# Kernel optimization log

Hardware: AMD Instinct MI355X
Metric: run time of the kernel (lower is better)

The kernel has to match this reference:

```python
import jax, jax.numpy as jnp
import numpy as np

T, E, IN_F, OUT_F = 16384, 8, 2048, 4096


def setup_inputs() -> dict:
    key = jax.random.key(0)
    k1, k2 = jax.random.split(key)
    input_tokens = jax.random.normal(k1, (T, IN_F), dtype=jnp.float32)
    # weight_stack[e] is [out_features, in_features]; forward does x_e @ W_e.T
    weight_stack = jax.random.normal(k2, (E, OUT_F, IN_F), dtype=jnp.float32) * (1.0 / np.sqrt(IN_F))
    # tokens are pre-sorted by expert; sizes must sum to total_tokens
    m_sizes = jnp.full((E,), T // E, dtype=jnp.int32)
    m_offsets = jnp.concatenate([
        jnp.zeros((1,), jnp.int32),
        jnp.cumsum(m_sizes)[:-1].astype(jnp.int32),
    ])
    return {
        "input_tokens": input_tokens,
        "weight_stack": weight_stack,
        "m_sizes": m_sizes,
        "m_offsets": m_offsets,
    }


def reference(input_tokens, weight_stack, m_sizes, m_offsets):
    # Grouped GEMM: for expert e, rows [off_e : off_e + m_e] of the output are
    #   input_tokens[off_e : off_e + m_e] @ weight_stack[e].T
    # lax.ragged_dot expects rhs of shape [groups, K, N]; weight_stack is [E, N, K],
    # so a stride-only swapaxes gives the logical transpose (no data movement),
    # mirroring the CUTLASS stride-based transpose avoidance.
    rhs = jnp.swapaxes(weight_stack, 1, 2)  # [E, in_features, out_features]
    out = jax.lax.ragged_dot(input_tokens, rhs, m_sizes)  # [T, out_features]
    return out
```

## Files before the change

kernel.cpp:

```cpp
#include <hip/hip_runtime.h>
#include <hip/hip_bf16.h>
#include <stdint.h>

#define T_TOK 16384
#define NEXP  8
#define KF    2048
#define NF    4096

#define BM  256
#define BN  256
#define BKT 64
#define KT  (KF / BKT)

typedef __bf16 bf16;
typedef __attribute__((ext_vector_type(8))) __bf16  bf16x8;
typedef __attribute__((ext_vector_type(4))) __bf16  bf16x4;
typedef __attribute__((ext_vector_type(4))) float   f32x4;

__device__ __forceinline__ void async_copy16(const void* g, void* l) {
  __builtin_amdgcn_global_load_lds(
      (const __attribute__((address_space(1))) void*)g,
      (__attribute__((address_space(3))) void*)l,
      16, 0, 0);
}

__global__ __launch_bounds__(256) void convert_f32_to_bf16(
    const float* __restrict__ in, bf16* __restrict__ out, int n8) {
  int i = blockIdx.x * 256 + threadIdx.x;
  if (i >= n8) return;
  const float4* p = (const float4*)(in + (size_t)i * 8);
  float4 a = p[0];
  float4 b = p[1];
  bf16x8 v;
  v[0] = (bf16)a.x; v[1] = (bf16)a.y; v[2] = (bf16)a.z; v[3] = (bf16)a.w;
  v[4] = (bf16)b.x; v[5] = (bf16)b.y; v[6] = (bf16)b.z; v[7] = (bf16)b.w;
  *(bf16x8*)(out + (size_t)i * 8) = v;
}

__global__ __launch_bounds__(512, 2) void grouped_gemm_8ph(
    const bf16* __restrict__ Xb, const bf16* __restrict__ Wb,
    const int* __restrict__ m_offsets, float* __restrict__ out)
{
  __shared__ bf16 As[2][BM * BKT];
  __shared__ bf16 Bs[2][BN * BKT];

  const int bid = blockIdx.x;
  const int swz = (bid & 7) * 128 + (bid >> 3);
  const int m0 = (swz >> 4) * BM;
  const int n0 = (swz & 15) * BN;

  int e = 0;
#pragma unroll
  for (int i = 1; i < NEXP; ++i)
    if (m0 >= m_offsets[i]) e = i;

  const int tid  = threadIdx.x;
  const int lane = tid & 63;
  const int wave = tid >> 6;
  const int wm = (wave >> 2) * 128;
  const int wn = (wave & 3) * 64;
  const int q  = lane >> 4;
  const int r  = lane & 15;

  const bf16* Ag = Xb + (size_t)m0 * KF;
  const bf16* Bg = Wb + ((size_t)e * NF + n0) * KF;

  const int crow = tid >> 3;
  const int cbs  = (((tid & 7) << 4) ^ ((crow & 7) << 4));

#define STAGE_A(BUF, H, TT) do {                                              \
    const bf16* _s = Ag + (size_t)((H) * 128 + crow) * KF + (TT) * BKT        \
                        + (cbs >> 1);                                         \
    char* _d = (char*)(&As[(BUF)][(H) * 128 * BKT]) + tid * 16;               \
    async_copy16(_s, _d);                                                     \
    async_copy16(_s + (size_t)64 * KF, _d + 8192);                            \
  } while (0)
#define STAGE_B(BUF, H, TT) do {                                              \
    const bf16* _s = Bg + (size_t)((H) * 128 + crow) * KF + (TT) * BKT        \
                        + (cbs >> 1);                                         \
    char* _d = (char*)(&Bs[(BUF)][(H) * 128 * BKT]) + tid * 16;               \
    async_copy16(_s, _d);                                                     \
    async_copy16(_s + (size_t)64 * KF, _d + 8192);                            \
  } while (0)

  f32x4 acc[8][4];
#pragma unroll
  for (int m = 0; m < 8; ++m)
#pragma unroll
    for (int n = 0; n < 4; ++n)
      acc[m][n] = (f32x4)0.0f;

  STAGE_A(0, 0, 0); STAGE_A(0, 1, 0); STAGE_B(0, 0, 0); STAGE_B(0, 1, 0);
  STAGE_B(1, 0, 1); STAGE_B(1, 1, 1); STAGE_A(1, 0, 1);
  asm volatile("s_waitcnt vmcnt(6)" ::: "memory");
  __builtin_amdgcn_s_barrier();
  __builtin_amdgcn_sched_barrier(0);

#pragma unroll 2
  for (int t = 0; t < KT; ++t) {
    const int buf = t & 1;
    const char* Ab = (const char*)&As[buf][0];
    const char* Bb = (const char*)&Bs[buf][0];
    bf16x8 b0[4], b1[4], al[4], ah[4];

#pragma unroll
    for (int n = 0; n < 4; ++n) {
      const int row = wn + n * 16 + r;
      b0[n] = *(const bf16x8*)(Bb + row * 128 + ((q * 16) ^ ((row & 7) << 4)));
    }
#pragma unroll
    for (int m = 0; m < 4; ++m) {
      const int row = wm + m * 16 + r;
      al[m] = *(const bf16x8*)(Ab + row * 128 + ((q * 16) ^ ((row & 7) << 4)));
    }
#pragma unroll
    for (int n = 0; n < 4; ++n) {
      const int row = wn + n * 16 + r;
      b1[n] = *(const bf16x8*)(Bb + row * 128 + ((64 + q * 16) ^ ((row & 7) << 4)));
    }
#pragma unroll
    for (int m = 0; m < 4; ++m) {
      const int row = wm + (4 + m) * 16 + r;
      ah[m] = *(const bf16x8*)(Ab + row * 128 + ((q * 16) ^ ((row & 7) << 4)));
    }
    if (t + 1 < KT) STAGE_A(buf ^ 1, 1, t + 1);
    __builtin_amdgcn_s_barrier();
    asm volatile("s_waitcnt lgkmcnt(0)" ::: "memory");
    __builtin_amdgcn_sched_barrier(0);
    __builtin_amdgcn_s_setprio(1);
#pragma unroll
    for (int m = 0; m < 4; ++m)
#pragma unroll
      for (int n = 0; n < 4; ++n)
        acc[m][n] = __builtin_amdgcn_mfma_f32_16x16x32_bf16(
            al[m], b0[n], acc[m][n], 0, 0, 0);
    __builtin_amdgcn_s_setprio(0);
    __builtin_amdgcn_s_barrier();

    if (t + 2 < KT) STAGE_B(buf, 0, t + 2);
    __builtin_amdgcn_s_barrier();
    __builtin_amdgcn_sched_barrier(0);
    __builtin_amdgcn_s_setprio(1);
#pragma unroll
    for (int m = 0; m < 4; ++m)
#pragma unroll
      for (int n = 0; n < 4; ++n)
        acc[4 + m][n] = __builtin_amdgcn_mfma_f32_16x16x32_bf16(
            ah[m], b0[n], acc[4 + m][n], 0, 0, 0);
    __builtin_amdgcn_s_setprio(0);
    __builtin_amdgcn_s_barrier();

#pragma unroll
    for (int m = 0; m < 4; ++m) {
      const int row = wm + m * 16 + r;
      al[m] = *(const bf16x8*)(Ab + row * 128 + ((64 + q * 16) ^ ((row & 7) << 4)));
    }
#pragma unroll
    for (int m = 0; m < 4; ++m) {
      const int row = wm + (4 + m) * 16 + r;
      ah[m] = *(const bf16x8*)(Ab + row * 128 + ((64 + q * 16) ^ ((row & 7) << 4)));
    }
    if (t + 2 < KT) STAGE_B(buf, 1, t + 2);
    __builtin_amdgcn_s_barrier();
    asm volatile("s_waitcnt lgkmcnt(0)" ::: "memory");
    __builtin_amdgcn_sched_barrier(0);
    __builtin_amdgcn_s_setprio(1);
#pragma unroll
    for (int m = 0; m < 4; ++m)
#pragma unroll
      for (int n = 0; n < 4; ++n)
        acc[m][n] = __builtin_amdgcn_mfma_f32_16x16x32_bf16(
            al[m], b1[n], acc[m][n], 0, 0, 0);
    __builtin_amdgcn_s_setprio(0);
    __builtin_amdgcn_s_barrier();

    if (t + 2 < KT) STAGE_A(buf, 0, t + 2);
    __builtin_amdgcn_s_barrier();
    __builtin_amdgcn_sched_barrier(0);
    __builtin_amdgcn_s_setprio(1);
#pragma unroll
    for (int m = 0; m < 4; ++m)
#pragma unroll
      for (int n = 0; n < 4; ++n)
        acc[4 + m][n] = __builtin_amdgcn_mfma_f32_16x16x32_bf16(
            ah[m], b1[n], acc[4 + m][n], 0, 0, 0);
    __builtin_amdgcn_s_setprio(0);
    if (t + 1 < KT) {
      if (t + 2 < KT) { asm volatile("s_waitcnt vmcnt(6)" ::: "memory"); }
      else            { asm volatile("s_waitcnt vmcnt(0)" ::: "memory"); }
      __builtin_amdgcn_s_barrier();
      __builtin_amdgcn_sched_barrier(0);
    }
  }
#undef STAGE_A
#undef STAGE_B

#pragma unroll
  for (int m = 0; m < 8; ++m) {
#pragma unroll
    for (int n = 0; n < 4; ++n) {
      const int col = n0 + wn + n * 16 + r;
#pragma unroll
      for (int rr = 0; rr < 4; ++rr) {
        const int row = m0 + wm + m * 16 + q * 4 + rr;
        out[(size_t)row * NF + col] = acc[m][n][rr];
      }
    }
  }
}

template <bool PRE>
__global__ __launch_bounds__(256) void grouped_gemm_bt(
    const float* __restrict__ Xf, const bf16* __restrict__ Xb,
    const float* __restrict__ Wf, const bf16* __restrict__ Wb,
    const int* __restrict__ m_offsets,
    float* __restrict__ out)
{
  __shared__ bf16 As[128 * 32];
  __shared__ bf16 Bs[128 * 32];

  const int n0 = blockIdx.x * 128;
  const int m0 = blockIdx.y * 128;

  int e = 0;
#pragma unroll
  for (int i = 1; i < NEXP; ++i)
    if (m0 >= m_offsets[i]) e = i;

  const int tid  = threadIdx.x;
  const int lane = tid & 63;
  const int wave = tid >> 6;
  const int wm = (wave >> 1) * 64;
  const int wn = (wave & 1) * 64;
  const int q  = lane >> 4;
  const int r  = lane & 15;

  f32x4 acc[4][4];
#pragma unroll
  for (int im = 0; im < 4; ++im)
#pragma unroll
    for (int in = 0; in < 4; ++in)
      acc[im][in] = (f32x4)0.0f;

  const float* Af = Xf + (size_t)m0 * KF;
  const float* Bf = Wf + ((size_t)e * NF + n0) * KF;

  for (int kt = 0; kt < KF / 32; ++kt) {
#pragma unroll
    for (int i = 0; i < 4; ++i) {
      int f   = (i * 256 + tid) * 4;
      int row = f >> 5;
      int kel = f & 31;
      float4 av = *(const float4*)(Af + (size_t)row * KF + kt * 32 + kel);
      float4 bv = *(const float4*)(Bf + (size_t)row * KF + kt * 32 + kel);
      bf16x4 a4, b4;
      a4[0] = (bf16)av.x; a4[1] = (bf16)av.y; a4[2] = (bf16)av.z; a4[3] = (bf16)av.w;
      b4[0] = (bf16)bv.x; b4[1] = (bf16)bv.y; b4[2] = (bf16)bv.z; b4[3] = (bf16)bv.w;
      *(bf16x4*)(As + f) = a4;
      *(bf16x4*)(Bs + f) = b4;
    }
    __syncthreads();

    bf16x8 afr[4], bfr[4];
#pragma unroll
    for (int im = 0; im < 4; ++im)
      afr[im] = *(const bf16x8*)&As[(wm + im * 16 + r) * 32 + q * 8];
#pragma unroll
    for (int in = 0; in < 4; ++in)
      bfr[in] = *(const bf16x8*)&Bs[(wn + in * 16 + r) * 32 + q * 8];

#pragma unroll
    for (int im = 0; im < 4; ++im)
#pragma unroll
      for (int in = 0; in < 4; ++in)
        acc[im][in] = __builtin_amdgcn_mfma_f32_16x16x32_bf16(
            afr[im], bfr[in], acc[im][in], 0, 0, 0);

    __syncthreads();
  }

#pragma unroll
  for (int im = 0; im < 4; ++im) {
#pragma unroll
    for (int in = 0; in < 4; ++in) {
      int col = n0 + wn + in * 16 + r;
#pragma unroll
      for (int rr = 0; rr < 4; ++rr) {
        int row = m0 + wm + im * 16 + q * 4 + rr;
        out[(size_t)row * NF + col] = acc[im][in][rr];
      }
    }
  }
}

extern "C" void kernel_launch(void* const* d_in, const int* in_sizes, int n_in,
                              void* d_out, int out_size, void* d_ws, size_t ws_size,
                              hipStream_t stream) {
  const float* X         = (const float*)d_in[0];
  const float* W         = (const float*)d_in[1];
  const int*   m_offsets = (const int*)d_in[3];
  float*       out       = (float*)d_out;

  const size_t xElems = (size_t)T_TOK * KF;
  const size_t wElems = (size_t)NEXP * NF * KF;
  const size_t needed = (xElems + wElems) * sizeof(bf16);

  if (ws_size >= needed) {
    bf16* Xb = (bf16*)d_ws;
    bf16* Wb = (bf16*)((char*)d_ws + xElems * sizeof(bf16));
    int n8x = (int)(xElems / 8);
    int n8w = (int)(wElems / 8);
    convert_f32_to_bf16<<<n8x / 256, 256, 0, stream>>>(X, Xb, n8x);
    convert_f32_to_bf16<<<n8w / 256, 256, 0, stream>>>(W, Wb, n8w);
    dim3 grid((T_TOK / BM) * (NF / BN));
    grouped_gemm_8ph<<<grid, 512, 0, stream>>>(Xb, Wb, m_offsets, out);
  } else {
    dim3 grid(NF / 128, T_TOK / 128);
    grouped_gemm_bt<false><<<grid, 256, 0, stream>>>(
        X, nullptr, W, nullptr, m_offsets, out);
  }
}
```

Measured before the change: 807.8 us.

## Restructure GEMM main loop to cut barriers and overlap LDS reads with MFMA

Reworks the software pipeline of the bf16 grouped GEMM kernel. It removes most per-phase workgroup barriers, uses partial lgkmcnt waits so LDS fragment loads for the next phase overlap the current MFMA block, and regroups the async global-to-LDS staging: both A halves are issued early, both B halves after one barrier. The goal is less barrier stall and better latency hiding. The risk is LDS hazards, since fewer barriers protect buffer reuse, plus different register pressure. The fallback f32 kernel is only renamed, with the template removed.

```diff
diff --git a/kernel.cpp b/kernel.cpp
--- a/kernel.cpp
+++ b/kernel.cpp
@@ -37,7 +37,7 @@
   *(bf16x8*)(out + (size_t)i * 8) = v;
 }
 
-__global__ __launch_bounds__(512, 2) void grouped_gemm_8ph(
+__global__ __launch_bounds__(512, 2) void grouped_gemm_pipe(
     const bf16* __restrict__ Xb, const bf16* __restrict__ Wb,
     const int* __restrict__ m_offsets, float* __restrict__ out)
 {
@@ -91,8 +91,8 @@
       acc[m][n] = (f32x4)0.0f;
 
   STAGE_A(0, 0, 0); STAGE_A(0, 1, 0); STAGE_B(0, 0, 0); STAGE_B(0, 1, 0);
-  STAGE_B(1, 0, 1); STAGE_B(1, 1, 1); STAGE_A(1, 0, 1);
-  asm volatile("s_waitcnt vmcnt(6)" ::: "memory");
+  STAGE_B(1, 0, 1); STAGE_B(1, 1, 1);
+  asm volatile("s_waitcnt vmcnt(4)" ::: "memory");
   __builtin_amdgcn_s_barrier();
   __builtin_amdgcn_sched_barrier(0);
 
@@ -101,7 +101,7 @@
     const int buf = t & 1;
     const char* Ab = (const char*)&As[buf][0];
     const char* Bb = (const char*)&Bs[buf][0];
-    bf16x8 b0[4], b1[4], al[4], ah[4];
+    bf16x8 b0[4], b1[4], a0[4], a1[4];
 
 #pragma unroll
     for (int n = 0; n < 4; ++n) {
@@ -111,8 +111,9 @@
 #pragma unroll
     for (int m = 0; m < 4; ++m) {
       const int row = wm + m * 16 + r;
-      al[m] = *(const bf16x8*)(Ab + row * 128 + ((q * 16) ^ ((row & 7) << 4)));
-    }
+      a0[m] = *(const bf16x8*)(Ab + row * 128 + ((q * 16) ^ ((row & 7) << 4)));
+    }
+    __builtin_amdgcn_sched_barrier(0);
 #pragma unroll
     for (int n = 0; n < 4; ++n) {
       const int row = wn + n * 16 + r;
@@ -120,12 +121,12 @@
     }
 #pragma unroll
     for (int m = 0; m < 4; ++m) {
-      const int row = wm + (4 + m) * 16 + r;
-      ah[m] = *(const bf16x8*)(Ab + row * 128 + ((q * 16) ^ ((row & 7) << 4)));
-    }
-    if (t + 1 < KT) STAGE_A(buf ^ 1, 1, t + 1);
-    __builtin_amdgcn_s_barrier();
-    asm volatile("s_waitcnt lgkmcnt(0)" ::: "memory");
+      const int row = wm + 64 + m * 16 + r;
+      a1[m] = *(const bf16x8*)(Ab + row * 128 + ((q * 16) ^ ((row & 7) << 4)));
+    }
+    if (t + 1 < KT) { STAGE_A(buf ^ 1, 0, t + 1); STAGE_A(buf ^ 1, 1, t + 1); }
+
+    asm volatile("s_waitcnt lgkmcnt(8)" ::: "memory");
     __builtin_amdgcn_sched_barrier(0);
     __builtin_amdgcn_s_setprio(1);
 #pragma unroll
@@ -133,12 +134,16 @@
 #pragma unroll
       for (int n = 0; n < 4; ++n)
         acc[m][n] = __builtin_amdgcn_mfma_f32_16x16x32_bf16(
-            al[m], b0[n], acc[m][n], 0, 0, 0);
+            a0[m], b0[n], acc[m][n], 0, 0, 0);
     __builtin_amdgcn_s_setprio(0);
-    __builtin_amdgcn_s_barrier();
-
-    if (t + 2 < KT) STAGE_B(buf, 0, t + 2);
-    __builtin_amdgcn_s_barrier();
+    __builtin_amdgcn_sched_barrier(0);
+
+#pragma unroll
+    for (int m = 0; m < 4; ++m) {
+      const int row = wm + m * 16 + r;
+      a0[m] = *(const bf16x8*)(Ab + row * 128 + ((64 + q * 16) ^ ((row & 7) << 4)));
+    }
+    asm volatile("s_waitcnt lgkmcnt(4)" ::: "memory");
     __builtin_amdgcn_sched_barrier(0);
     __builtin_amdgcn_s_setprio(1);
 #pragma unroll
@@ -146,23 +151,16 @@
 #pragma unroll
       for (int n = 0; n < 4; ++n)
         acc[4 + m][n] = __builtin_amdgcn_mfma_f32_16x16x32_bf16(
-            ah[m], b0[n], acc[4 + m][n], 0, 0, 0);
+            a1[m], b0[n], acc[4 + m][n], 0, 0, 0);
     __builtin_amdgcn_s_setprio(0);
-    __builtin_amdgcn_s_barrier();
+    __builtin_amdgcn_sched_barrier(0);
 
 #pragma unroll
     for (int m = 0; m < 4; ++m) {
-      const int row = wm + m * 16 + r;
-      al[m] = *(const bf16x8*)(Ab + row * 128 + ((64 + q * 16) ^ ((row & 7) << 4)));
-    }
-#pragma unroll
-    for (int m = 0; m < 4; ++m) {
-      const int row = wm + (4 + m) * 16 + r;
-      ah[m] = *(const bf16x8*)(Ab + row * 128 + ((64 + q * 16) ^ ((row & 7) << 4)));
-    }
-    if (t + 2 < KT) STAGE_B(buf, 1, t + 2);
-    __builtin_amdgcn_s_barrier();
-    asm volatile("s_waitcnt lgkmcnt(0)" ::: "memory");
+      const int row = wm + 64 + m * 16 + r;
+      a1[m] = *(const bf16x8*)(Ab + row * 128 + ((64 + q * 16) ^ ((row & 7) << 4)));
+    }
+    asm volatile("s_waitcnt lgkmcnt(4)" ::: "memory");
     __builtin_amdgcn_sched_barrier(0);
     __builtin_amdgcn_s_setprio(1);
 #pragma unroll
@@ -170,12 +168,13 @@
 #pragma unroll
       for (int n = 0; n < 4; ++n)
         acc[m][n] = __builtin_amdgcn_mfma_f32_16x16x32_bf16(
-            al[m], b1[n], acc[m][n], 0, 0, 0);
+            a0[m], b1[n], acc[m][n], 0, 0, 0);
     __builtin_amdgcn_s_setprio(0);
+
     __builtin_amdgcn_s_barrier();
-
-    if (t + 2 < KT) STAGE_A(buf, 0, t + 2);
-    __builtin_amdgcn_s_barrier();
+    if (t + 2 < KT) { STAGE_B(buf, 0, t + 2); STAGE_B(buf, 1, t + 2); }
+
+    asm volatile("s_waitcnt lgkmcnt(0)" ::: "memory");
     __builtin_amdgcn_sched_barrier(0);
     __builtin_amdgcn_s_setprio(1);
 #pragma unroll
@@ -183,10 +182,11 @@
 #pragma unroll
       for (int n = 0; n < 4; ++n)
         acc[4 + m][n] = __builtin_amdgcn_mfma_f32_16x16x32_bf16(
-            ah[m], b1[n], acc[4 + m][n], 0, 0, 0);
+            a1[m], b1[n], acc[4 + m][n], 0, 0, 0);
     __builtin_amdgcn_s_setprio(0);
+
     if (t + 1 < KT) {
-      if (t + 2 < KT) { asm volatile("s_waitcnt vmcnt(6)" ::: "memory"); }
+      if (t + 2 < KT) { asm volatile("s_waitcnt vmcnt(4)" ::: "memory"); }
       else            { asm volatile("s_waitcnt vmcnt(0)" ::: "memory"); }
       __builtin_amdgcn_s_barrier();
       __builtin_amdgcn_sched_barrier(0);
@@ -209,12 +209,9 @@
   }
 }
 
-template <bool PRE>
-__global__ __launch_bounds__(256) void grouped_gemm_bt(
-    const float* __restrict__ Xf, const bf16* __restrict__ Xb,
-    const float* __restrict__ Wf, const bf16* __restrict__ Wb,
-    const int* __restrict__ m_offsets,
-    float* __restrict__ out)
+__global__ __launch_bounds__(256) void grouped_gemm_bt_f32(
+    const float* __restrict__ Xf, const float* __restrict__ Wf,
+    const int* __restrict__ m_offsets, float* __restrict__ out)
 {
   __shared__ bf16 As[128 * 32];
   __shared__ bf16 Bs[128 * 32];
@@ -313,10 +310,10 @@
     convert_f32_to_bf16<<<n8x / 256, 256, 0, stream>>>(X, Xb, n8x);
     convert_f32_to_bf16<<<n8w / 256, 256, 0, stream>>>(W, Wb, n8w);
     dim3 grid((T_TOK / BM) * (NF / BN));
-    grouped_gemm_8ph<<<grid, 512, 0, stream>>>(Xb, Wb, m_offsets, out);
+    grouped_gemm_pipe<<<grid, 512, 0, stream>>>(Xb, Wb, m_offsets, out);
   } else {
     dim3 grid(NF / 128, T_TOK / 128);
-    grouped_gemm_bt<false><<<grid, 256, 0, stream>>>(
-        X, nullptr, W, nullptr, m_offsets, out);
-  }
-}
+    grouped_gemm_bt_f32<<<grid, 256, 0, stream>>>(
+        X, W, m_offsets, out);
+  }
+}
```

Measured after the change: 776.9 us. 3.8% less time.
